# Kernel optimization log

Measured on AMD Instinct MI355X. Metric: run time of the kernel, lower is better.

The kernel has to match this reference:

```python
import jax, jax.numpy as jnp
import numpy as np

BS, L, NPH, NQ, H = 64, 512, 16, 16, 1024
EPS = 1e-5

def _ln(x, g, b):
    m = jnp.mean(x, axis=-1, keepdims=True)
    v = jnp.mean((x - m) ** 2, axis=-1, keepdims=True)
    return (x - m) * jax.lax.rsqrt(v + EPS) * g + b

def setup_inputs() -> dict:
    key = jax.random.key(0)
    ks = jax.random.split(key, 24)
    s = 0.02
    inp = {
        "lang_context_feat": jax.random.normal(ks[0], (BS, L, H), jnp.float32),
        "lang_query_feat": jax.random.normal(ks[1], (BS, NPH, H), jnp.float32),
        "mask_query_context": jax.random.randint(ks[2], (BS, NPH, L), 0, 2).astype(bool),
        "query_embed": jax.random.normal(ks[3], (NQ, 2 * H), jnp.float32) * s,
        # linear1/2/3: hidden -> hidden (stored [in, out])
        "W1": jax.random.normal(ks[4], (H, H), jnp.float32) * s, "b1": jnp.zeros((H,), jnp.float32),
        "W2": jax.random.normal(ks[5], (H, H), jnp.float32) * s, "b2": jnp.zeros((H,), jnp.float32),
        "W3": jax.random.normal(ks[6], (H, H), jnp.float32) * s, "b3": jnp.zeros((H,), jnp.float32),
        # context_out: Linear(h,h) + LayerNorm(h)
        "Wc": jax.random.normal(ks[7], (H, H), jnp.float32) * s, "bc": jnp.zeros((H,), jnp.float32),
        "gc": jnp.ones((H,), jnp.float32), "betac": jnp.zeros((H,), jnp.float32),
        # fuse_encoder_query: Linear(2h,h)+LN+ReLU+Dropout(eval)+Linear(h,h)+LN+ReLU
        "Wf1": jax.random.normal(ks[8], (2 * H, H), jnp.float32) * s, "bf1": jnp.zeros((H,), jnp.float32),
        "gf1": jnp.ones((H,), jnp.float32), "betaf1": jnp.zeros((H,), jnp.float32),
        "Wf2": jax.random.normal(ks[9], (H, H), jnp.float32) * s, "bf2": jnp.zeros((H,), jnp.float32),
        "gf2": jnp.ones((H,), jnp.float32), "betaf2": jnp.zeros((H,), jnp.float32),
    }
    return inp

def reference(lang_context_feat, lang_query_feat, mask_query_context,
              query_embed, W1, b1, W2, b2, W3, b3,
              Wc, bc, gc, betac,
              Wf1, bf1, gf1, betaf1, Wf2, bf2, gf2, betaf2):
    # single-query attention: k from first context token, q/v from all tokens
    k = lang_context_feat[:, 0:1, :] @ W1 + b1          # [bs,1,h]
    q = lang_context_feat @ W2 + b2                     # [bs,L,h]
    v = lang_context_feat @ W3 + b3                     # [bs,L,h]
    att = jnp.einsum("bih,blh->bil", k, q)             # [bs,1,L]
    att = jnp.broadcast_to(att, mask_query_context.shape)  # [bs,n_ph,L]
    att = jnp.where(mask_query_context, -jnp.inf, att)
    p = jax.nn.softmax(att, axis=-1)                    # [bs,n_ph,L]
    ctx = jnp.einsum("bpl,blh->bph", p, v)             # [bs,n_ph,h]
    ctx = _ln(ctx @ Wc + bc, gc, betac)
    ctx = lang_context_feat[:, None, 0, :] + ctx        # residual with first token
    x = jnp.concatenate([ctx, lang_query_feat], axis=-1)   # [bs,n_ph,2h]
    x = jax.nn.relu(_ln(x @ Wf1 + bf1, gf1, betaf1))        # dropout: eval mode (identity)
    x = jax.nn.relu(_ln(x @ Wf2 + bf2, gf2, betaf2))        # [bs,n_ph,h]
    # repeat(1,1,1,2) on last dim == tile [x, x]
    pq = jnp.concatenate([x, x], axis=-1)[:, :, None, :]    # [bs,n_ph,1,2h]
    pq = pq + query_embed[None, None, :, :]                 # [bs,n_ph,n_q,2h]
    pq = pq.reshape(pq.shape[0], -1, 2 * H).transpose(1, 0, 2)  # [n_ph*n_q,bs,2h]
    return pq[..., :H], pq[..., H:]
```

## Files before the change

### kernel.cpp

```cpp
#include <hip/hip_runtime.h>

typedef __bf16 bf16;
typedef __bf16 bf16x8 __attribute__((ext_vector_type(8)));
typedef __bf16 bf16x4 __attribute__((ext_vector_type(4)));
typedef float f32x4 __attribute__((ext_vector_type(4)));

#define LCTX 512
#define HD 1024

__device__ __forceinline__ float wave_sum(float v) {
    for (int off = 32; off; off >>= 1) v += __shfl_xor(v, off, 64);
    return v;
}
__device__ __forceinline__ float wave_max(float v) {
    for (int off = 32; off; off >>= 1) v = fmaxf(v, __shfl_xor(v, off, 64));
    return v;
}

__global__ __launch_bounds__(256) void prep_kernel(const float* __restrict__ W3,
                                                   const float* __restrict__ Wc,
                                                   const float* __restrict__ Wf1,
                                                   const float* __restrict__ Wf2,
                                                   const float* __restrict__ lq,
                                                   const float* __restrict__ x,
                                                   const float* __restrict__ W1,
                                                   bf16* __restrict__ W3t, bf16* __restrict__ Wct,
                                                   bf16* __restrict__ Wf1t, bf16* __restrict__ Wf2t,
                                                   bf16* __restrict__ X,
                                                   float* __restrict__ kpartial) {
    __shared__ __align__(16) char smem[33792];
    int blk = blockIdx.x, t = threadIdx.x;
    if (blk < 5120) {
        float (*tile)[33] = (float(*)[33])smem;
        const float* W; bf16* Wt; int K, N, i;
        if (blk < 1024)      { W = W3;  Wt = W3t;  K = 1024; N = 1024; i = blk; }
        else if (blk < 2048) { W = Wc;  Wt = Wct;  K = 1024; N = 1024; i = blk - 1024; }
        else if (blk < 3072) { W = Wf2; Wt = Wf2t; K = 1024; N = 1024; i = blk - 2048; }
        else                 { W = Wf1; Wt = Wf1t; K = 2048; N = 1024; i = blk - 3072; }
        int k0 = (i >> 5) * 32, n0 = (i & 31) * 32;
        int c = t & 31, r = t >> 5;
#pragma unroll
        for (int j = 0; j < 4; j++)
            tile[r + j * 8][c] = W[(size_t)(k0 + r + j * 8) * N + n0 + c];
        __syncthreads();
#pragma unroll
        for (int j = 0; j < 4; j++)
            Wt[(size_t)(n0 + r + j * 8) * K + k0 + c] = (bf16)tile[c][r + j * 8];
    } else if (blk < 6144) {
        int i = (blk - 5120) * 256 + t;
        float4 v = ((const float4*)lq)[i];
        int row = i >> 8, h4 = i & 255;
        bf16x4 o = {(bf16)v.x, (bf16)v.y, (bf16)v.z, (bf16)v.w};
        *(bf16x4*)(X + (size_t)row * 2048 + 1024 + h4 * 4) = o;
    } else {
        float (*xs)[68] = (float(*)[68])smem;
        float (*wsm)[64] = (float(*)[64])(smem + 17408);
        int kv = blk - 6144;
        int n0 = (kv & 15) * 64, k0 = (kv >> 4) * 64;
#pragma unroll
        for (int i = 0; i < 4; i++) {
            int f = t + i * 256;
            int b = f >> 4, c = f & 15;
            *(float4*)&xs[b][c * 4] =
                *(const float4*)(x + (size_t)b * LCTX * HD + k0 + c * 4);
        }
#pragma unroll
        for (int i = 0; i < 4; i++) {
            int f = t + i * 256;
            int r = f >> 4, c = f & 15;
            *(float4*)&wsm[r][c * 4] =
                *(const float4*)(W1 + (size_t)(k0 + r) * 1024 + n0 + c * 4);
        }
        __syncthreads();
        int tb = t >> 4, tc = t & 15;
        int b0 = tb * 4;
        float acc[4][4] = {};
        for (int kk = 0; kk < 64; kk += 4) {
            float4 w0 = *(const float4*)&wsm[kk + 0][tc * 4];
            float4 w1 = *(const float4*)&wsm[kk + 1][tc * 4];
            float4 w2 = *(const float4*)&wsm[kk + 2][tc * 4];
            float4 w3 = *(const float4*)&wsm[kk + 3][tc * 4];
            float4 xv[4];
#pragma unroll
            for (int bi = 0; bi < 4; bi++) xv[bi] = *(const float4*)&xs[b0 + bi][kk];
#pragma unroll
            for (int bi = 0; bi < 4; bi++) {
                acc[bi][0] += xv[bi].x * w0.x + xv[bi].y * w1.x + xv[bi].z * w2.x + xv[bi].w * w3.x;
                acc[bi][1] += xv[bi].x * w0.y + xv[bi].y * w1.y + xv[bi].z * w2.y + xv[bi].w * w3.y;
                acc[bi][2] += xv[bi].x * w0.z + xv[bi].y * w1.z + xv[bi].z * w2.z + xv[bi].w * w3.z;
                acc[bi][3] += xv[bi].x * w0.w + xv[bi].y * w1.w + xv[bi].z * w2.w + xv[bi].w * w3.w;
            }
        }
        float* pout = kpartial + ((size_t)(kv >> 4) * 64 + b0) * 1024 + n0 + tc * 4;
#pragma unroll
        for (int bi = 0; bi < 4; bi++)
            *(float4*)(pout + (size_t)bi * 1024) =
                make_float4(acc[bi][0], acc[bi][1], acc[bi][2], acc[bi][3]);
    }
}

__global__ __launch_bounds__(256) void mmat_kernel(const float* __restrict__ partial,
                                                   const float* __restrict__ b1,
                                                   const float* __restrict__ W2,
                                                   float* __restrict__ mout) {
    __shared__ float ks[1024];
    int b = blockIdx.x, i0 = blockIdx.y * 64, t = threadIdx.x;
    {
        float4 acc = ((const float4*)b1)[t];
#pragma unroll
        for (int kt = 0; kt < 16; kt++) {
            float4 v = ((const float4*)(partial + ((size_t)kt * 64 + b) * 1024))[t];
            acc.x += v.x; acc.y += v.y; acc.z += v.z; acc.w += v.w;
        }
        *(float4*)&ks[t * 4] = acc;
    }
    __syncthreads();
    int wave = t >> 6, lane = t & 63;
    for (int rr = 0; rr < 16; rr++) {
        int i = i0 + wave * 16 + rr;
        const float* wrow = W2 + (size_t)i * 1024;
        float s = 0.f;
#pragma unroll
        for (int j = 0; j < 4; j++) {
            float4 wv = ((const float4*)wrow)[lane + j * 64];
            const float4 kv = *(const float4*)&ks[(lane + j * 64) * 4];
            s += wv.x * kv.x + wv.y * kv.y + wv.z * kv.z + wv.w * kv.w;
        }
        s = wave_sum(s);
        if (lane == 0) mout[(size_t)b * 1024 + i] = s;
    }
}

__global__ __launch_bounds__(256) void att_kernel(const float* __restrict__ x,
                                                  const float* __restrict__ m,
                                                  float* __restrict__ att) {
    __shared__ float ms[1024];
    int b = blockIdx.x, l0 = blockIdx.y * 32, t = threadIdx.x;
    *(float4*)&ms[t * 4] = ((const float4*)(m + (size_t)b * 1024))[t];
    __syncthreads();
    int wave = t >> 6, lane = t & 63;
    for (int rr = 0; rr < 8; rr++) {
        int l = l0 + wave * 8 + rr;
        const float* xr = x + ((size_t)b * LCTX + l) * HD;
        float s = 0.f;
#pragma unroll
        for (int j = 0; j < 4; j++) {
            float4 xv = ((const float4*)xr)[lane + j * 64];
            const float4 mv = *(const float4*)&ms[(lane + j * 64) * 4];
            s += xv.x * mv.x + xv.y * mv.y + xv.z * mv.z + xv.w * mv.w;
        }
        s = wave_sum(s);
        if (lane == 0) att[(size_t)b * LCTX + l] = s;
    }
}

__global__ __launch_bounds__(256) void ypart_kernel(const float* __restrict__ att,
                                                    const unsigned char* __restrict__ mask,
                                                    const float* __restrict__ x,
                                                    float* __restrict__ ypartial) {
    __shared__ float ps[16][128];
    __shared__ float att_s[512];
    __shared__ int sstr;
    int b = blockIdx.x, lqi = blockIdx.y, t = threadIdx.x;
    int l0 = lqi * 128;
    int wave = t >> 6, lane = t & 63;
    if (t == 0) sstr = 4;
    if (t < 128) ((float4*)att_s)[t] = ((const float4*)(att + (size_t)b * LCTX))[t];
    __syncthreads();
    if (t < 128 && ((const unsigned int*)mask)[t] > 1u) sstr = 1;
    __syncthreads();
    int stride = sstr;
#pragma unroll
    for (int q = 0; q < 4; q++) {
        int pp = wave * 4 + q;
        size_t mbase = ((size_t)(b * 16 + pp)) * LCTX;
        float av[8];
#pragma unroll
        for (int j = 0; j < 8; j++) {
            int l = lane + j * 64;
            bool mk = mask[(mbase + l) * (size_t)stride] != 0;
            av[j] = mk ? -1e30f : att_s[l];
        }
        float mx = av[0];
#pragma unroll
        for (int j = 1; j < 8; j++) mx = fmaxf(mx, av[j]);
        mx = wave_max(mx);
        float s = 0.f;
#pragma unroll
        for (int j = 0; j < 8; j++) {
            av[j] = (av[j] <= -1e29f) ? 0.f : expf(av[j] - mx);
            s += av[j];
        }
        s = wave_sum(s);
        float inv = 1.f / s;
#pragma unroll
        for (int j = 0; j < 8; j++) {
            int l = lane + j * 64;
            if (l >= l0 && l < l0 + 128) ps[pp][l - l0] = av[j] * inv;
        }
    }
    __syncthreads();
    float4 acc[16];
#pragma unroll
    for (int q = 0; q < 16; q++) acc[q] = make_float4(0.f, 0.f, 0.f, 0.f);
    const float4* xb = (const float4*)(x + ((size_t)b * LCTX + l0) * HD) + t;
    for (int l = 0; l < 128; l++) {
        float4 xv = xb[(size_t)l * 256];
#pragma unroll
        for (int q = 0; q < 16; q++) {
            float pv = ps[q][l];
            acc[q].x += pv * xv.x; acc[q].y += pv * xv.y;
            acc[q].z += pv * xv.z; acc[q].w += pv * xv.w;
        }
    }
    float* yp = ypartial + ((size_t)lqi * 1024 + b * 16) * 1024 + t * 4;
#pragma unroll
    for (int q = 0; q < 16; q++)
        *(float4*)(yp + (size_t)q * 1024) = acc[q];
}

__global__ __launch_bounds__(256) void yred_kernel(const float* __restrict__ ypartial,
                                                   bf16* __restrict__ y) {
    int i = blockIdx.x * 256 + threadIdx.x;
    float4 a0 = ((const float4*)ypartial)[i];
    float4 a1 = ((const float4*)(ypartial + (size_t)1 * 1024 * 1024))[i];
    float4 a2 = ((const float4*)(ypartial + (size_t)2 * 1024 * 1024))[i];
    float4 a3 = ((const float4*)(ypartial + (size_t)3 * 1024 * 1024))[i];
    float sx = a0.x + a1.x + a2.x + a3.x;
    float sy = a0.y + a1.y + a2.y + a3.y;
    float sz = a0.z + a1.z + a2.z + a3.z;
    float sw = a0.w + a1.w + a2.w + a3.w;
    bf16x4 o = {(bf16)sx, (bf16)sy, (bf16)sz, (bf16)sw};
    *(bf16x4*)(y + (size_t)i * 4) = o;
}

__device__ __forceinline__ void gl16(const bf16* g, bf16* l) {
    __builtin_amdgcn_global_load_lds((const __attribute__((address_space(1))) void*)g,
                                     (__attribute__((address_space(3))) void*)l, 16, 0, 0);
}
__device__ __forceinline__ bf16x8 ldsfrag(const bf16* base, int row, int kb) {
    return *(const bf16x8*)(base + row * 64 + ((kb ^ (row & 7)) << 3));
}

template <bool OUT_BF16>
__global__ __launch_bounds__(256) void gemm_kernel(const bf16* __restrict__ A, int lda,
                                                   const bf16* __restrict__ Bt, int ldb,
                                                   const float* __restrict__ bias,
                                                   void* __restrict__ Cv, int ldc, int K) {
    __shared__ bf16 sA[2][4096];
    __shared__ bf16 sB[2][4096];
    int tid = threadIdx.x;
    int wave = tid >> 6, lane = tid & 63;
    int m0 = blockIdx.x * 64, n0 = blockIdx.y * 64;
    int wr = (wave >> 1) * 32, wc = (wave & 1) * 32;
    int l16 = lane & 15, lhi = lane >> 4;
    int r0 = tid >> 3, kb = tid & 7;
    int r1 = r0 + 32;
    int sk0 = (kb ^ (r0 & 7)) << 3;
    int sk1 = (kb ^ (r1 & 7)) << 3;
    const bf16* A0 = A + (size_t)(m0 + r0) * lda + sk0;
    const bf16* A1 = A + (size_t)(m0 + r1) * lda + sk1;
    const bf16* B0 = Bt + (size_t)(n0 + r0) * ldb + sk0;
    const bf16* B1 = Bt + (size_t)(n0 + r1) * ldb + sk1;
    int wb0 = (wave * 64) * 8;
    int wb1 = (256 + wave * 64) * 8;

    f32x4 acc00 = {}, acc01 = {}, acc10 = {}, acc11 = {};

    int nt = K >> 6;
    gl16(A0, &sA[0][wb0]); gl16(A1, &sA[0][wb1]);
    gl16(B0, &sB[0][wb0]); gl16(B1, &sB[0][wb1]);
    asm volatile("s_waitcnt vmcnt(0)" ::: "memory");
    __syncthreads();
    int cur = 0;
    for (int tI = 0; tI < nt; ++tI) {
        if (tI + 1 < nt) {
            int ko = (tI + 1) << 6;
            gl16(A0 + ko, &sA[cur ^ 1][wb0]); gl16(A1 + ko, &sA[cur ^ 1][wb1]);
            gl16(B0 + ko, &sB[cur ^ 1][wb0]); gl16(B1 + ko, &sB[cur ^ 1][wb1]);
        }
        const bf16* a = sA[cur];
        const bf16* bt = sB[cur];
#pragma unroll
        for (int ks = 0; ks < 2; ks++) {
            int kbb = ks * 4 + lhi;
            bf16x8 a0 = ldsfrag(a, wr + l16, kbb);
            bf16x8 a1v = ldsfrag(a, wr + 16 + l16, kbb);
            bf16x8 b0v = ldsfrag(bt, wc + l16, kbb);
            bf16x8 b1v = ldsfrag(bt, wc + 16 + l16, kbb);
            acc00 = __builtin_amdgcn_mfma_f32_16x16x32_bf16(a0, b0v, acc00, 0, 0, 0);
            acc01 = __builtin_amdgcn_mfma_f32_16x16x32_bf16(a0, b1v, acc01, 0, 0, 0);
            acc10 = __builtin_amdgcn_mfma_f32_16x16x32_bf16(a1v, b0v, acc10, 0, 0, 0);
            acc11 = __builtin_amdgcn_mfma_f32_16x16x32_bf16(a1v, b1v, acc11, 0, 0, 0);
        }
        asm volatile("s_waitcnt vmcnt(0)" ::: "memory");
        __syncthreads();
        cur ^= 1;
    }
    f32x4 accs[2][2] = {{acc00, acc01}, {acc10, acc11}};
#pragma unroll
    for (int mi = 0; mi < 2; mi++)
#pragma unroll
        for (int ni = 0; ni < 2; ni++)
#pragma unroll
            for (int r = 0; r < 4; r++) {
                int row = m0 + wr + mi * 16 + lhi * 4 + r;
                int col = n0 + wc + ni * 16 + l16;
                float v = accs[mi][ni][r] + bias[col];
                if (OUT_BF16)
                    ((bf16*)Cv)[(size_t)row * ldc + col] = (bf16)v;
                else
                    ((float*)Cv)[(size_t)row * ldc + col] = v;
            }
}

template <int MODE>
__global__ __launch_bounds__(256) void ln_kernel(const float* __restrict__ C,
                                                 const float* __restrict__ g,
                                                 const float* __restrict__ beta,
                                                 const float* __restrict__ resid,
                                                 void* __restrict__ out) {
    __shared__ float r1[8], r2[8];
    int row = blockIdx.x, t = threadIdx.x;
    float4 v = ((const float4*)(C + (size_t)row * 1024))[t];
    float s = v.x + v.y + v.z + v.w;
    float s2 = v.x * v.x + v.y * v.y + v.z * v.z + v.w * v.w;
    s = wave_sum(s); s2 = wave_sum(s2);
    int wave = t >> 6, lane = t & 63;
    if (lane == 0) { r1[wave] = s; r2[wave] = s2; }
    __syncthreads();
    float S = r1[0] + r1[1] + r1[2] + r1[3];
    float S2 = r2[0] + r2[1] + r2[2] + r2[3];
    float mean = S * (1.f / 1024.f);
    float var = S2 * (1.f / 1024.f) - mean * mean;
    float inv = rsqrtf(var + 1e-5f);
    float4 gv = ((const float4*)g)[t];
    float4 bv = ((const float4*)beta)[t];
    float o[4];
    o[0] = (v.x - mean) * inv * gv.x + bv.x;
    o[1] = (v.y - mean) * inv * gv.y + bv.y;
    o[2] = (v.z - mean) * inv * gv.z + bv.z;
    o[3] = (v.w - mean) * inv * gv.w + bv.w;
    if (MODE == 0) {
        int b = row >> 4;
        const float* x0 = resid + (size_t)b * LCTX * HD + t * 4;
        bf16x4 w = {(bf16)(o[0] + x0[0]), (bf16)(o[1] + x0[1]),
                    (bf16)(o[2] + x0[2]), (bf16)(o[3] + x0[3])};
        *(bf16x4*)((bf16*)out + (size_t)row * 2048 + t * 4) = w;
    } else {
        bf16x4 w = {(bf16)fmaxf(o[0], 0.f), (bf16)fmaxf(o[1], 0.f),
                    (bf16)fmaxf(o[2], 0.f), (bf16)fmaxf(o[3], 0.f)};
        *(bf16x4*)((bf16*)out + (size_t)row * 1024 + t * 4) = w;
    }
}

__global__ __launch_bounds__(256) void lnout_kernel(const float* __restrict__ C,
                                                    const float* __restrict__ g,
                                                    const float* __restrict__ beta,
                                                    const float* __restrict__ qe,
                                                    float* __restrict__ out) {
    __shared__ float r1[8], r2[8];
    int row = blockIdx.x, t = threadIdx.x;
    int b = row >> 4, pp = row & 15;
    float4 v = ((const float4*)(C + (size_t)row * 1024))[t];
    float s = v.x + v.y + v.z + v.w;
    float s2 = v.x * v.x + v.y * v.y + v.z * v.z + v.w * v.w;
    s = wave_sum(s); s2 = wave_sum(s2);
    int wave = t >> 6, lane = t & 63;
    if (lane == 0) { r1[wave] = s; r2[wave] = s2; }
    __syncthreads();
    float S = r1[0] + r1[1] + r1[2] + r1[3];
    float S2 = r2[0] + r2[1] + r2[2] + r2[3];
    float mean = S * (1.f / 1024.f);
    float var = S2 * (1.f / 1024.f) - mean * mean;
    float inv = rsqrtf(var + 1e-5f);
    float4 gv = ((const float4*)g)[t];
    float4 bv = ((const float4*)beta)[t];
    float4 ov;
    ov.x = fmaxf((v.x - mean) * inv * gv.x + bv.x, 0.f);
    ov.y = fmaxf((v.y - mean) * inv * gv.y + bv.y, 0.f);
    ov.z = fmaxf((v.z - mean) * inv * gv.z + bv.z, 0.f);
    ov.w = fmaxf((v.w - mean) * inv * gv.w + bv.w, 0.f);
    float* out0 = out;
    float* out1 = out + (size_t)256 * 64 * 1024;
#pragma unroll
    for (int q = 0; q < 16; q++) {
        float4 q0 = ((const float4*)(qe + (size_t)q * 2048))[t];
        float4 q1 = ((const float4*)(qe + (size_t)q * 2048 + 1024))[t];
        size_t orow = ((size_t)(pp * 16 + q) * 64 + b) * 1024;
        ((float4*)(out0 + orow))[t] =
            make_float4(ov.x + q0.x, ov.y + q0.y, ov.z + q0.z, ov.w + q0.w);
        ((float4*)(out1 + orow))[t] =
            make_float4(ov.x + q1.x, ov.y + q1.y, ov.z + q1.z, ov.w + q1.w);
    }
}

extern "C" void kernel_launch(void* const* d_in, const int* in_sizes, int n_in,
                              void* d_out, int out_size, void* d_ws, size_t ws_size,
                              hipStream_t stream) {
    const float* x      = (const float*)d_in[0];
    const float* lq     = (const float*)d_in[1];
    const unsigned char* mask = (const unsigned char*)d_in[2];
    const float* qe     = (const float*)d_in[3];
    const float* W1     = (const float*)d_in[4];
    const float* b1     = (const float*)d_in[5];
    const float* W2     = (const float*)d_in[6];
    const float* W3     = (const float*)d_in[8];
    const float* b3     = (const float*)d_in[9];
    const float* Wc     = (const float*)d_in[10];
    const float* bc     = (const float*)d_in[11];
    const float* gc     = (const float*)d_in[12];
    const float* betac  = (const float*)d_in[13];
    const float* Wf1    = (const float*)d_in[14];
    const float* bf1    = (const float*)d_in[15];
    const float* gf1    = (const float*)d_in[16];
    const float* betaf1 = (const float*)d_in[17];
    const float* Wf2    = (const float*)d_in[18];
    const float* bf2    = (const float*)d_in[19];
    const float* gf2    = (const float*)d_in[20];
    const float* betaf2 = (const float*)d_in[21];

    char* ws = (char*)d_ws;
    const size_t MB = 1 << 20;
    bf16* W3t   = (bf16*)(ws + 0 * MB);
    bf16* Wct   = (bf16*)(ws + 2 * MB);
    bf16* Wf1t  = (bf16*)(ws + 4 * MB);
    bf16* Wf2t  = (bf16*)(ws + 8 * MB);
    bf16* X     = (bf16*)(ws + 10 * MB);
    float* mbuf = (float*)(ws + 14 * MB + 256 * 1024);
    float* attb = (float*)(ws + 14 * MB + 512 * 1024);
    bf16* ybuf  = (bf16*)(ws + 17 * MB);
    bf16* ctxp  = (bf16*)(ws + 19 * MB);
    float* Cbuf = (float*)(ws + 21 * MB);
    bf16* t1    = (bf16*)(ws + 25 * MB);
    float* ypartial = (float*)(ws + 32 * MB);
    float* kpartial = Cbuf;

    prep_kernel<<<6400, 256, 0, stream>>>(W3, Wc, Wf1, Wf2, lq, x, W1,
                                          W3t, Wct, Wf1t, Wf2t, X, kpartial);
    mmat_kernel<<<dim3(64, 16), 256, 0, stream>>>(kpartial, b1, W2, mbuf);
    att_kernel<<<dim3(64, 16), 256, 0, stream>>>(x, mbuf, attb);
    ypart_kernel<<<dim3(64, 4), 256, 0, stream>>>(attb, mask, x, ypartial);
    yred_kernel<<<1024, 256, 0, stream>>>(ypartial, ybuf);
    gemm_kernel<true><<<dim3(16, 16), 256, 0, stream>>>(ybuf, 1024, W3t, 1024, b3,
                                                        ctxp, 1024, 1024);
    gemm_kernel<false><<<dim3(16, 16), 256, 0, stream>>>(ctxp, 1024, Wct, 1024, bc,
                                                         Cbuf, 1024, 1024);
    ln_kernel<0><<<1024, 256, 0, stream>>>(Cbuf, gc, betac, x, X);
    gemm_kernel<false><<<dim3(16, 16), 256, 0, stream>>>(X, 2048, Wf1t, 2048, bf1,
                                                         Cbuf, 1024, 2048);
    ln_kernel<1><<<1024, 256, 0, stream>>>(Cbuf, gf1, betaf1, nullptr, t1);
    gemm_kernel<false><<<dim3(16, 16), 256, 0, stream>>>(t1, 1024, Wf2t, 1024, bf2,
                                                         Cbuf, 1024, 1024);
    lnout_kernel<<<1024, 256, 0, stream>>>(Cbuf, gf2, betaf2, qe, (float*)d_out);
}
```

Measured before the change: 241.3 us.

## Fuse LayerNorm into GEMM prologue/epilogue and split attention-weighted sum finer

```diff
diff --git a/kernel.cpp b/kernel.cpp
--- a/kernel.cpp
+++ b/kernel.cpp
@@ -21,13 +21,13 @@
                                                    const float* __restrict__ Wc,
                                                    const float* __restrict__ Wf1,
                                                    const float* __restrict__ Wf2,
-                                                   const float* __restrict__ lq,
                                                    const float* __restrict__ x,
                                                    const float* __restrict__ W1,
                                                    bf16* __restrict__ W3t, bf16* __restrict__ Wct,
                                                    bf16* __restrict__ Wf1t, bf16* __restrict__ Wf2t,
-                                                   bf16* __restrict__ X,
-                                                   float* __restrict__ kpartial) {
+                                                   float* __restrict__ kpartial,
+                                                   float* __restrict__ stats1,
+                                                   float* __restrict__ stats2) {
     __shared__ __align__(16) char smem[33792];
     int blk = blockIdx.x, t = threadIdx.x;
     if (blk < 5120) {
@@ -46,16 +46,10 @@
 #pragma unroll
         for (int j = 0; j < 4; j++)
             Wt[(size_t)(n0 + r + j * 8) * K + k0 + c] = (bf16)tile[c][r + j * 8];
-    } else if (blk < 6144) {
-        int i = (blk - 5120) * 256 + t;
-        float4 v = ((const float4*)lq)[i];
-        int row = i >> 8, h4 = i & 255;
-        bf16x4 o = {(bf16)v.x, (bf16)v.y, (bf16)v.z, (bf16)v.w};
-        *(bf16x4*)(X + (size_t)row * 2048 + 1024 + h4 * 4) = o;
-    } else {
+    } else if (blk < 5376) {
         float (*xs)[68] = (float(*)[68])smem;
         float (*wsm)[64] = (float(*)[64])(smem + 17408);
-        int kv = blk - 6144;
+        int kv = blk - 5120;
         int n0 = (kv & 15) * 64, k0 = (kv >> 4) * 64;
 #pragma unroll
         for (int i = 0; i < 4; i++) {
@@ -96,6 +90,12 @@
         for (int bi = 0; bi < 4; bi++)
             *(float4*)(pout + (size_t)bi * 1024) =
                 make_float4(acc[bi][0], acc[bi][1], acc[bi][2], acc[bi][3]);
+    } else {
+        float4 z = make_float4(0.f, 0.f, 0.f, 0.f);
+        for (int i = t; i < 512; i += 256) {
+            ((float4*)stats1)[i] = z;
+            ((float4*)stats2)[i] = z;
+        }
     }
 }
 
@@ -158,11 +158,11 @@
                                                     const unsigned char* __restrict__ mask,
                                                     const float* __restrict__ x,
                                                     float* __restrict__ ypartial) {
-    __shared__ float ps[16][128];
+    __shared__ float ps[16][64];
     __shared__ float att_s[512];
     __shared__ int sstr;
     int b = blockIdx.x, lqi = blockIdx.y, t = threadIdx.x;
-    int l0 = lqi * 128;
+    int l0 = lqi * 64;
     int wave = t >> 6, lane = t & 63;
     if (t == 0) sstr = 4;
     if (t < 128) ((float4*)att_s)[t] = ((const float4*)(att + (size_t)b * LCTX))[t];
@@ -192,45 +192,44 @@
             s += av[j];
         }
         s = wave_sum(s);
-        float inv = 1.f / s;
-#pragma unroll
-        for (int j = 0; j < 8; j++) {
-            int l = lane + j * 64;
-            if (l >= l0 && l < l0 + 128) ps[pp][l - l0] = av[j] * inv;
-        }
-    }
-    __syncthreads();
-    float4 acc[16];
-#pragma unroll
-    for (int q = 0; q < 16; q++) acc[q] = make_float4(0.f, 0.f, 0.f, 0.f);
+        float sel = av[0];
+#pragma unroll
+        for (int j = 1; j < 8; j++) if (lqi == j) sel = av[j];
+        ps[pp][lane] = sel * (1.f / s);
+    }
+    __syncthreads();
+    f32x4 acc[16] = {};
     const float4* xb = (const float4*)(x + ((size_t)b * LCTX + l0) * HD) + t;
-    for (int l = 0; l < 128; l++) {
-        float4 xv = xb[(size_t)l * 256];
+    for (int l4 = 0; l4 < 64; l4 += 4) {
+        float4 xv0 = xb[(size_t)(l4 + 0) * 256];
+        float4 xv1 = xb[(size_t)(l4 + 1) * 256];
+        float4 xv2 = xb[(size_t)(l4 + 2) * 256];
+        float4 xv3 = xb[(size_t)(l4 + 3) * 256];
 #pragma unroll
         for (int q = 0; q < 16; q++) {
-            float pv = ps[q][l];
-            acc[q].x += pv * xv.x; acc[q].y += pv * xv.y;
-            acc[q].z += pv * xv.z; acc[q].w += pv * xv.w;
+            float4 pv = *(const float4*)&ps[q][l4];
+            acc[q].x += pv.x * xv0.x + pv.y * xv1.x + pv.z * xv2.x + pv.w * xv3.x;
+            acc[q].y += pv.x * xv0.y + pv.y * xv1.y + pv.z * xv2.y + pv.w * xv3.y;
+            acc[q].z += pv.x * xv0.z + pv.y * xv1.z + pv.z * xv2.z + pv.w * xv3.z;
+            acc[q].w += pv.x * xv0.w + pv.y * xv1.w + pv.z * xv2.w + pv.w * xv3.w;
         }
     }
     float* yp = ypartial + ((size_t)lqi * 1024 + b * 16) * 1024 + t * 4;
 #pragma unroll
     for (int q = 0; q < 16; q++)
-        *(float4*)(yp + (size_t)q * 1024) = acc[q];
+        *(f32x4*)(yp + (size_t)q * 1024) = acc[q];
 }
 
 __global__ __launch_bounds__(256) void yred_kernel(const float* __restrict__ ypartial,
                                                    bf16* __restrict__ y) {
     int i = blockIdx.x * 256 + threadIdx.x;
-    float4 a0 = ((const float4*)ypartial)[i];
-    float4 a1 = ((const float4*)(ypartial + (size_t)1 * 1024 * 1024))[i];
-    float4 a2 = ((const float4*)(ypartial + (size_t)2 * 1024 * 1024))[i];
-    float4 a3 = ((const float4*)(ypartial + (size_t)3 * 1024 * 1024))[i];
-    float sx = a0.x + a1.x + a2.x + a3.x;
-    float sy = a0.y + a1.y + a2.y + a3.y;
-    float sz = a0.z + a1.z + a2.z + a3.z;
-    float sw = a0.w + a1.w + a2.w + a3.w;
-    bf16x4 o = {(bf16)sx, (bf16)sy, (bf16)sz, (bf16)sw};
+    float4 s = ((const float4*)ypartial)[i];
+#pragma unroll
+    for (int c = 1; c < 8; c++) {
+        float4 v = ((const float4*)(ypartial + (size_t)c * 1024 * 1024))[i];
+        s.x += v.x; s.y += v.y; s.z += v.z; s.w += v.w;
+    }
+    bf16x4 o = {(bf16)s.x, (bf16)s.y, (bf16)s.z, (bf16)s.w};
     *(bf16x4*)(y + (size_t)i * 4) = o;
 }
 
@@ -242,11 +241,62 @@
     return *(const bf16x8*)(base + row * 64 + ((kb ^ (row & 7)) << 3));
 }
 
-template <bool OUT_BF16>
-__global__ __launch_bounds__(256) void gemm_kernel(const bf16* __restrict__ A, int lda,
-                                                   const bf16* __restrict__ Bt, int ldb,
-                                                   const float* __restrict__ bias,
-                                                   void* __restrict__ Cv, int ldc, int K) {
+template <int AMODE>
+__device__ __forceinline__ bf16x8 stage_ln(const float* __restrict__ Af,
+                                           const float* __restrict__ lqf,
+                                           int row, int lk, float mean, float inv,
+                                           const float* __restrict__ g,
+                                           const float* __restrict__ bta,
+                                           const float* __restrict__ x0row) {
+    float4 c0, c1;
+    if (lk < 1024) {
+        c0 = *(const float4*)(Af + (size_t)row * 1024 + lk);
+        c1 = *(const float4*)(Af + (size_t)row * 1024 + lk + 4);
+        float4 g0 = *(const float4*)(g + lk);
+        float4 g1 = *(const float4*)(g + lk + 4);
+        float4 t0 = *(const float4*)(bta + lk);
+        float4 t1 = *(const float4*)(bta + lk + 4);
+        c0.x = (c0.x - mean) * inv * g0.x + t0.x;
+        c0.y = (c0.y - mean) * inv * g0.y + t0.y;
+        c0.z = (c0.z - mean) * inv * g0.z + t0.z;
+        c0.w = (c0.w - mean) * inv * g0.w + t0.w;
+        c1.x = (c1.x - mean) * inv * g1.x + t1.x;
+        c1.y = (c1.y - mean) * inv * g1.y + t1.y;
+        c1.z = (c1.z - mean) * inv * g1.z + t1.z;
+        c1.w = (c1.w - mean) * inv * g1.w + t1.w;
+        if (AMODE == 1) {
+            float4 r0v = *(const float4*)(x0row + lk);
+            float4 r1v = *(const float4*)(x0row + lk + 4);
+            c0.x += r0v.x; c0.y += r0v.y; c0.z += r0v.z; c0.w += r0v.w;
+            c1.x += r1v.x; c1.y += r1v.y; c1.z += r1v.z; c1.w += r1v.w;
+        } else {
+            c0.x = fmaxf(c0.x, 0.f); c0.y = fmaxf(c0.y, 0.f);
+            c0.z = fmaxf(c0.z, 0.f); c0.w = fmaxf(c0.w, 0.f);
+            c1.x = fmaxf(c1.x, 0.f); c1.y = fmaxf(c1.y, 0.f);
+            c1.z = fmaxf(c1.z, 0.f); c1.w = fmaxf(c1.w, 0.f);
+        }
+    } else {
+        c0 = *(const float4*)(lqf + (size_t)row * 1024 + lk - 1024);
+        c1 = *(const float4*)(lqf + (size_t)row * 1024 + lk - 1024 + 4);
+    }
+    bf16x8 o = {(bf16)c0.x, (bf16)c0.y, (bf16)c0.z, (bf16)c0.w,
+                (bf16)c1.x, (bf16)c1.y, (bf16)c1.z, (bf16)c1.w};
+    return o;
+}
+
+template <int AMODE, bool STATS, bool OUT_BF16>
+__global__ __launch_bounds__(256) void gemm_kernel(
+    const bf16* __restrict__ A, int lda,
+    const float* __restrict__ Af,
+    const float* __restrict__ lqf,
+    const float* __restrict__ lnstats,
+    const float* __restrict__ lng,
+    const float* __restrict__ lnbeta,
+    const float* __restrict__ x0base,
+    const bf16* __restrict__ Bt, int ldb,
+    const float* __restrict__ bias,
+    void* __restrict__ Cv, int ldc, int K,
+    float* __restrict__ stats_out) {
     __shared__ bf16 sA[2][4096];
     __shared__ bf16 sB[2][4096];
     int tid = threadIdx.x;
@@ -256,27 +306,57 @@
     int l16 = lane & 15, lhi = lane >> 4;
     int r0 = tid >> 3, kb = tid & 7;
     int r1 = r0 + 32;
-    int sk0 = (kb ^ (r0 & 7)) << 3;
-    int sk1 = (kb ^ (r1 & 7)) << 3;
-    const bf16* A0 = A + (size_t)(m0 + r0) * lda + sk0;
-    const bf16* A1 = A + (size_t)(m0 + r1) * lda + sk1;
-    const bf16* B0 = Bt + (size_t)(n0 + r0) * ldb + sk0;
-    const bf16* B1 = Bt + (size_t)(n0 + r1) * ldb + sk1;
-    int wb0 = (wave * 64) * 8;
-    int wb1 = (256 + wave * 64) * 8;
+    int pk0 = (kb ^ (r0 & 7)) << 3;
+    int pk1 = (kb ^ (r1 & 7)) << 3;
+    const bf16* B0 = Bt + (size_t)(n0 + r0) * ldb + pk0;
+    const bf16* B1 = Bt + (size_t)(n0 + r1) * ldb + pk1;
+    int wb0 = wave * 512, wb1 = 2048 + wave * 512;
+
+    const bf16* A0 = nullptr; const bf16* A1 = nullptr;
+    float mean0 = 0.f, inv0 = 0.f, mean1 = 0.f, inv1 = 0.f;
+    const float* x0r0 = nullptr; const float* x0r1 = nullptr;
+    if (AMODE == 0) {
+        A0 = A + (size_t)(m0 + r0) * lda + pk0;
+        A1 = A + (size_t)(m0 + r1) * lda + pk1;
+    } else {
+        float s = lnstats[(m0 + r0) * 2], s2 = lnstats[(m0 + r0) * 2 + 1];
+        mean0 = s * (1.f / 1024.f);
+        inv0 = rsqrtf(s2 * (1.f / 1024.f) - mean0 * mean0 + 1e-5f);
+        s = lnstats[(m0 + r1) * 2]; s2 = lnstats[(m0 + r1) * 2 + 1];
+        mean1 = s * (1.f / 1024.f);
+        inv1 = rsqrtf(s2 * (1.f / 1024.f) - mean1 * mean1 + 1e-5f);
+        if (AMODE == 1) {
+            x0r0 = x0base + (size_t)((m0 + r0) >> 4) * LCTX * HD;
+            x0r1 = x0base + (size_t)((m0 + r1) >> 4) * LCTX * HD;
+        }
+    }
 
     f32x4 acc00 = {}, acc01 = {}, acc10 = {}, acc11 = {};
-
     int nt = K >> 6;
-    gl16(A0, &sA[0][wb0]); gl16(A1, &sA[0][wb1]);
+
+    if (AMODE == 0) {
+        gl16(A0, &sA[0][wb0]); gl16(A1, &sA[0][wb1]);
+    } else {
+        bf16x8 a0 = stage_ln<AMODE>(Af, lqf, m0 + r0, kb * 8, mean0, inv0, lng, lnbeta, x0r0);
+        bf16x8 a1 = stage_ln<AMODE>(Af, lqf, m0 + r1, kb * 8, mean1, inv1, lng, lnbeta, x0r1);
+        *(bf16x8*)&sA[0][r0 * 64 + pk0] = a0;
+        *(bf16x8*)&sA[0][r1 * 64 + pk1] = a1;
+    }
     gl16(B0, &sB[0][wb0]); gl16(B1, &sB[0][wb1]);
     asm volatile("s_waitcnt vmcnt(0)" ::: "memory");
     __syncthreads();
     int cur = 0;
     for (int tI = 0; tI < nt; ++tI) {
-        if (tI + 1 < nt) {
+        bf16x8 a0n, a1n;
+        bool nxt = (tI + 1 < nt);
+        if (nxt) {
             int ko = (tI + 1) << 6;
-            gl16(A0 + ko, &sA[cur ^ 1][wb0]); gl16(A1 + ko, &sA[cur ^ 1][wb1]);
+            if (AMODE == 0) {
+                gl16(A0 + ko, &sA[cur ^ 1][wb0]); gl16(A1 + ko, &sA[cur ^ 1][wb1]);
+            } else {
+                a0n = stage_ln<AMODE>(Af, lqf, m0 + r0, ko + kb * 8, mean0, inv0, lng, lnbeta, x0r0);
+                a1n = stage_ln<AMODE>(Af, lqf, m0 + r1, ko + kb * 8, mean1, inv1, lng, lnbeta, x0r1);
+            }
             gl16(B0 + ko, &sB[cur ^ 1][wb0]); gl16(B1 + ko, &sB[cur ^ 1][wb1]);
         }
         const bf16* a = sA[cur];
@@ -293,6 +373,10 @@
             acc10 = __builtin_amdgcn_mfma_f32_16x16x32_bf16(a1v, b0v, acc10, 0, 0, 0);
             acc11 = __builtin_amdgcn_mfma_f32_16x16x32_bf16(a1v, b1v, acc11, 0, 0, 0);
         }
+        if (AMODE != 0 && nxt) {
+            *(bf16x8*)&sA[cur ^ 1][r0 * 64 + pk0] = a0n;
+            *(bf16x8*)&sA[cur ^ 1][r1 * 64 + pk1] = a1n;
+        }
         asm volatile("s_waitcnt vmcnt(0)" ::: "memory");
         __syncthreads();
         cur ^= 1;
@@ -301,57 +385,31 @@
 #pragma unroll
     for (int mi = 0; mi < 2; mi++)
 #pragma unroll
-        for (int ni = 0; ni < 2; ni++)
-#pragma unroll
-            for (int r = 0; r < 4; r++) {
-                int row = m0 + wr + mi * 16 + lhi * 4 + r;
+        for (int r = 0; r < 4; r++) {
+            int row = m0 + wr + mi * 16 + lhi * 4 + r;
+            float vsum = 0.f, vsq = 0.f;
+#pragma unroll
+            for (int ni = 0; ni < 2; ni++) {
                 int col = n0 + wc + ni * 16 + l16;
                 float v = accs[mi][ni][r] + bias[col];
                 if (OUT_BF16)
                     ((bf16*)Cv)[(size_t)row * ldc + col] = (bf16)v;
                 else
                     ((float*)Cv)[(size_t)row * ldc + col] = v;
+                vsum += v; vsq += v * v;
             }
-}
-
-template <int MODE>
-__global__ __launch_bounds__(256) void ln_kernel(const float* __restrict__ C,
-                                                 const float* __restrict__ g,
-                                                 const float* __restrict__ beta,
-                                                 const float* __restrict__ resid,
-                                                 void* __restrict__ out) {
-    __shared__ float r1[8], r2[8];
-    int row = blockIdx.x, t = threadIdx.x;
-    float4 v = ((const float4*)(C + (size_t)row * 1024))[t];
-    float s = v.x + v.y + v.z + v.w;
-    float s2 = v.x * v.x + v.y * v.y + v.z * v.z + v.w * v.w;
-    s = wave_sum(s); s2 = wave_sum(s2);
-    int wave = t >> 6, lane = t & 63;
-    if (lane == 0) { r1[wave] = s; r2[wave] = s2; }
-    __syncthreads();
-    float S = r1[0] + r1[1] + r1[2] + r1[3];
-    float S2 = r2[0] + r2[1] + r2[2] + r2[3];
-    float mean = S * (1.f / 1024.f);
-    float var = S2 * (1.f / 1024.f) - mean * mean;
-    float inv = rsqrtf(var + 1e-5f);
-    float4 gv = ((const float4*)g)[t];
-    float4 bv = ((const float4*)beta)[t];
-    float o[4];
-    o[0] = (v.x - mean) * inv * gv.x + bv.x;
-    o[1] = (v.y - mean) * inv * gv.y + bv.y;
-    o[2] = (v.z - mean) * inv * gv.z + bv.z;
-    o[3] = (v.w - mean) * inv * gv.w + bv.w;
-    if (MODE == 0) {
-        int b = row >> 4;
-        const float* x0 = resid + (size_t)b * LCTX * HD + t * 4;
-        bf16x4 w = {(bf16)(o[0] + x0[0]), (bf16)(o[1] + x0[1]),
-                    (bf16)(o[2] + x0[2]), (bf16)(o[3] + x0[3])};
-        *(bf16x4*)((bf16*)out + (size_t)row * 2048 + t * 4) = w;
-    } else {
-        bf16x4 w = {(bf16)fmaxf(o[0], 0.f), (bf16)fmaxf(o[1], 0.f),
-                    (bf16)fmaxf(o[2], 0.f), (bf16)fmaxf(o[3], 0.f)};
-        *(bf16x4*)((bf16*)out + (size_t)row * 1024 + t * 4) = w;
-    }
+            if (STATS) {
+#pragma unroll
+                for (int off = 1; off < 16; off <<= 1) {
+                    vsum += __shfl_xor(vsum, off, 64);
+                    vsq  += __shfl_xor(vsq, off, 64);
+                }
+                if (l16 == 0) {
+                    atomicAdd(&stats_out[row * 2], vsum);
+                    atomicAdd(&stats_out[row * 2 + 1], vsq);
+                }
+            }
+        }
 }
 
 __global__ __launch_bounds__(256) void lnout_kernel(const float* __restrict__ C,
@@ -422,35 +480,38 @@
 
     char* ws = (char*)d_ws;
     const size_t MB = 1 << 20;
-    bf16* W3t   = (bf16*)(ws + 0 * MB);
-    bf16* Wct   = (bf16*)(ws + 2 * MB);
-    bf16* Wf1t  = (bf16*)(ws + 4 * MB);
-    bf16* Wf2t  = (bf16*)(ws + 8 * MB);
-    bf16* X     = (bf16*)(ws + 10 * MB);
-    float* mbuf = (float*)(ws + 14 * MB + 256 * 1024);
-    float* attb = (float*)(ws + 14 * MB + 512 * 1024);
-    bf16* ybuf  = (bf16*)(ws + 17 * MB);
-    bf16* ctxp  = (bf16*)(ws + 19 * MB);
-    float* Cbuf = (float*)(ws + 21 * MB);
-    bf16* t1    = (bf16*)(ws + 25 * MB);
+    bf16* W3t    = (bf16*)(ws + 0 * MB);
+    bf16* Wct    = (bf16*)(ws + 2 * MB);
+    bf16* Wf1t   = (bf16*)(ws + 4 * MB);
+    bf16* Wf2t   = (bf16*)(ws + 8 * MB);
+    float* mbuf  = (float*)(ws + 14 * MB + 256 * 1024);
+    float* attb  = (float*)(ws + 14 * MB + 512 * 1024);
+    float* stats1 = (float*)(ws + 15 * MB);
+    float* stats2 = (float*)(ws + 15 * MB + 64 * 1024);
+    bf16* ybuf   = (bf16*)(ws + 17 * MB);
+    bf16* ctxp   = (bf16*)(ws + 19 * MB);
+    float* Cbuf  = (float*)(ws + 21 * MB);
+    float* Cbuf2 = (float*)(ws + 25 * MB);
     float* ypartial = (float*)(ws + 32 * MB);
     float* kpartial = Cbuf;
 
-    prep_kernel<<<6400, 256, 0, stream>>>(W3, Wc, Wf1, Wf2, lq, x, W1,
-                                          W3t, Wct, Wf1t, Wf2t, X, kpartial);
+    prep_kernel<<<5377, 256, 0, stream>>>(W3, Wc, Wf1, Wf2, x, W1,
+                                          W3t, Wct, Wf1t, Wf2t, kpartial, stats1, stats2);
     mmat_kernel<<<dim3(64, 16), 256, 0, stream>>>(kpartial, b1, W2, mbuf);
     att_kernel<<<dim3(64, 16), 256, 0, stream>>>(x, mbuf, attb);
-    ypart_kernel<<<dim3(64, 4), 256, 0, stream>>>(attb, mask, x, ypartial);
+    ypart_kernel<<<dim3(64, 8), 256, 0, stream>>>(attb, mask, x, ypartial);
     yred_kernel<<<1024, 256, 0, stream>>>(ypartial, ybuf);
-    gemm_kernel<true><<<dim3(16, 16), 256, 0, stream>>>(ybuf, 1024, W3t, 1024, b3,
-                                                        ctxp, 1024, 1024);
-    gemm_kernel<false><<<dim3(16, 16), 256, 0, stream>>>(ctxp, 1024, Wct, 1024, bc,
-                                                         Cbuf, 1024, 1024);
-    ln_kernel<0><<<1024, 256, 0, stream>>>(Cbuf, gc, betac, x, X);
-    gemm_kernel<false><<<dim3(16, 16), 256, 0, stream>>>(X, 2048, Wf1t, 2048, bf1,
-                                                         Cbuf, 1024, 2048);
-    ln_kernel<1><<<1024, 256, 0, stream>>>(Cbuf, gf1, betaf1, nullptr, t1);
-    gemm_kernel<false><<<dim3(16, 16), 256, 0, stream>>>(t1, 1024, Wf2t, 1024, bf2,
-                                                         Cbuf, 1024, 1024);
+    gemm_kernel<0, false, true><<<dim3(16, 16), 256, 0, stream>>>(
+        ybuf, 1024, nullptr, nullptr, nullptr, nullptr, nullptr, nullptr,
+        W3t, 1024, b3, ctxp, 1024, 1024, nullptr);
+    gemm_kernel<0, true, false><<<dim3(16, 16), 256, 0, stream>>>(
+        ctxp, 1024, nullptr, nullptr, nullptr, nullptr, nullptr, nullptr,
+        Wct, 1024, bc, Cbuf, 1024, 1024, stats1);
+    gemm_kernel<1, true, false><<<dim3(16, 16), 256, 0, stream>>>(
+        nullptr, 0, Cbuf, lq, stats1, gc, betac, x,
+        Wf1t, 2048, bf1, Cbuf2, 1024, 2048, stats2);
+    gemm_kernel<2, false, false><<<dim3(16, 16), 256, 0, stream>>>(
+        nullptr, 0, Cbuf2, nullptr, stats2, gf1, betaf1, nullptr,
+        Wf2t, 1024, bf2, Cbuf, 1024, 1024, nullptr);
     lnout_kernel<<<1024, 256, 0, stream>>>(Cbuf, gf2, betaf2, qe, (float*)d_out);
 }
```

Result: slower. 307.2 us (+27.3%).
